# Kernel tuning notes

Measured on AMD Instinct MI355X. Metric: run time of the kernel, lower is better.

Reference implementation:

```python
import jax, jax.numpy as jnp
import numpy as np

B, T, D, L, K = 4, 2048, 2048, 2048, 4  # batch, seq, width, lru_width, conv temporal width


def setup_inputs() -> dict:
    key = jax.random.key(0)
    ks = jax.random.split(key, 12)
    s = 0.02
    f32 = jnp.float32
    return {
        "x": jax.random.normal(ks[0], (B, T, D), f32),
        "w_y": jax.random.normal(ks[1], (D, L), f32) * s,
        "b_y": jnp.zeros((L,), f32),
        "w_x": jax.random.normal(ks[2], (D, L), f32) * s,
        "b_x": jnp.zeros((L,), f32),
        "conv_w": jax.random.normal(ks[3], (K, L), f32) * s,
        "conv_b": jnp.zeros((L,), f32),
        "a_param": jax.random.uniform(ks[4], (L,), f32, 0.5, 4.0),
        "w_ig": jax.random.normal(ks[5], (L, L), f32) * s,
        "b_ig": jnp.zeros((L,), f32),
        "w_ag": jax.random.normal(ks[6], (L, L), f32) * s,
        "b_ag": jnp.zeros((L,), f32),
        "w_out": jax.random.normal(ks[7], (L, D), f32) * s,
        "b_out": jnp.zeros((D,), f32),
    }


def reference(x, w_y, b_y, w_x, b_x, conv_w, conv_b, a_param,
              w_ig, b_ig, w_ag, b_ag, w_out, b_out):
    # x: [B, T, D] (batch_first=True)
    Tn = x.shape[1]
    # gate branch: GELU(linear_y(x))
    y = jax.nn.gelu(jnp.einsum('btd,dl->btl', x, w_y) + b_y, approximate=False)
    # recurrent branch: linear_x -> causal depthwise conv1d (width K)
    xb = jnp.einsum('btd,dl->btl', x, w_x) + b_x
    xp = jnp.pad(xb, ((0, 0), (K - 1, 0), (0, 0)))  # zero left pad (fresh cache)
    conv = conv_b
    for k in range(K):  # y_t = b + sum_k w[k] * x_{t-(K-1-k)}
        conv = conv + conv_w[k] * xp[:, k:k + Tn]
    # RG-LRU
    gate_x = jax.nn.sigmoid(jnp.einsum('btl,lm->btm', conv, w_ig) + b_ig)
    gate_a = jax.nn.sigmoid(jnp.einsum('btl,lm->btm', conv, w_ag) + b_ag)
    log_a = -8.0 * gate_a * jax.nn.softplus(a_param)  # [B,T,L]
    a = jnp.exp(log_a)
    mult = jnp.sqrt(1.0 - jnp.exp(2.0 * log_a))
    reset = (jnp.arange(Tn) == 0)[None, :, None]  # reset at sequence start
    a = jnp.where(reset, 0.0, a)
    mult = jnp.where(reset, 1.0, mult)
    nx = gate_x * conv * mult
    # linear diagonal scan h_t = a_t * h_{t-1} + nx_t
    def step(h, inp):
        a_t, x_t = inp
        h = a_t * h + x_t
        return h, h
    h0 = jnp.zeros((x.shape[0], a.shape[-1]), x.dtype)
    hn, hs = jax.lax.scan(step, h0, (a.transpose(1, 0, 2), nx.transpose(1, 0, 2)))
    h_seq = hs.transpose(1, 0, 2)  # [B,T,L]
    out = jnp.einsum('btl,ld->btd', h_seq * y, w_out) + b_out
    return out, hn
```

## Files before the change

kernel.cpp:

```cpp
#include <hip/hip_runtime.h>
#include <math.h>

#define B_ 4
#define T_ 2048
#define D_ 2048
#define L_ 2048
#define KW 4
#define M_ (B_*T_)

typedef unsigned short u16;
typedef unsigned short u16x8 __attribute__((ext_vector_type(8)));
typedef __bf16 bf16x8 __attribute__((ext_vector_type(8)));
typedef float f32x4 __attribute__((ext_vector_type(4)));

__device__ __forceinline__ u16 f2bf(float f) {
    unsigned u = __float_as_uint(f);
    u += 0x7fffu + ((u >> 16) & 1u);
    return (u16)(u >> 16);
}
__device__ __forceinline__ float bf2f(u16 h) {
    return __uint_as_float(((unsigned)h) << 16);
}
__device__ __forceinline__ float gelu_exact(float v) {
    return 0.5f * v * (1.0f + erff(v * 0.70710678118654752440f));
}
__device__ __forceinline__ float sigmoidf_(float v) {
    return 1.0f / (1.0f + __expf(-v));
}
__device__ __forceinline__ void gload16(const void* g, void* l) {
    __builtin_amdgcn_global_load_lds(
        (const __attribute__((address_space(1))) void*)g,
        (__attribute__((address_space(3))) void*)l,
        16, 0, 0);
}
__device__ __forceinline__ void bar() {
    __builtin_amdgcn_s_barrier();
}

__global__ __launch_bounds__(256)
void castx_kernel(const float* __restrict__ in, u16* __restrict__ out)
{
    const int i = blockIdx.x * 256 + threadIdx.x;
    float4 v = ((const float4*)in)[i];
    ushort4 o;
    o.x = f2bf(v.x); o.y = f2bf(v.y); o.z = f2bf(v.z); o.w = f2bf(v.w);
    ((ushort4*)out)[i] = o;
}

__global__ __launch_bounds__(256)
void transcast_kernel(const float* __restrict__ in, u16* __restrict__ out,
                      int Kd, int Nd)
{
    __shared__ float tile[32][33];
    const int bx = blockIdx.x;
    const int by = blockIdx.y;
    const int tx = threadIdx.x & 31;
    const int ty = threadIdx.x >> 5;
    #pragma unroll
    for (int j = 0; j < 4; ++j) {
        const int r = by*32 + ty + j*8;
        tile[ty + j*8][tx] = in[(size_t)r * Nd + bx*32 + tx];
    }
    __syncthreads();
    #pragma unroll
    for (int j = 0; j < 4; ++j) {
        const int n = bx*32 + ty + j*8;
        out[(size_t)n * Kd + by*32 + tx] = f2bf(tile[tx][ty + j*8]);
    }
}

__device__ __forceinline__ void store_out(float* C, size_t idx, float v) { C[idx] = v; }
__device__ __forceinline__ void store_out(u16*   C, size_t idx, float v) { C[idx] = f2bf(v); }

template<int EPI, typename OutT>
__global__ __launch_bounds__(512, 4)
void mgemm_kernel(const u16* __restrict__ A, const u16* __restrict__ BT,
                  const float* __restrict__ bias, OutT* __restrict__ C,
                  int M, int N, int K,
                  const u16* __restrict__ auxA,
                  const u16* __restrict__ auxC,
                  const float* __restrict__ ap)
{
    __shared__ __align__(16) u16 lds[36864];
    u16* ldsB = lds + 24576;

    const int tid  = threadIdx.x;
    const int wave = tid >> 6;
    const int lane = tid & 63;

    const int nbx = N >> 7;
    const int nwg = nbx * (M >> 8);
    const int bid = blockIdx.x;
    const int li  = (bid & 7) * (nwg >> 3) + (bid >> 3);
    const int bm  = (li / nbx) * 256;
    const int bn  = (li % nbx) * 128;

    const int wr = wave >> 1;
    const int wn = wave & 1;
    const int lr = lane & 15;
    const int q  = lane >> 4;

    const int grow  = lane >> 2;
    const int gslot = (lane & 3) ^ ((lane >> 3) & 3);
    const u16* gA0 = A  + (size_t)(bm + wave*16     + grow) * K + gslot*8;
    const u16* gA1 = A  + (size_t)(bm + (wave+8)*16 + grow) * K + gslot*8;
    const u16* gB0 = BT + (size_t)(bn + wave*16     + grow) * K + gslot*8;
    const int dA0 = wave*512     + lane*8;
    const int dA1 = (wave+8)*512 + lane*8;
    const int dB0 = wave*512     + lane*8;

    auto STAGE = [&](int g) {
        const int s = g % 3;
        const size_t kg = (size_t)g << 5;
        u16* a = lds  + s*8192;
        u16* b = ldsB + s*4096;
        gload16(gA0 + kg, &a[dA0]);
        gload16(gA1 + kg, &a[dA1]);
        gload16(gB0 + kg, &b[dB0]);
    };

    const int ksw = (q ^ ((lr >> 1) & 3)) * 8;

    f32x4 acc[4][4] = {};

    STAGE(0); STAGE(1);
    asm volatile("s_waitcnt vmcnt(3)" ::: "memory");
    bar();

    const int NT = K >> 5;
    for (int g = 0; g < NT; ++g) {
        const int s = g % 3;
        const u16* Ab = lds  + s*8192;
        const u16* Bb = ldsB + s*4096;

        bf16x8 a[4], b[4];
        #pragma unroll
        for (int i = 0; i < 4; ++i)
            a[i] = *(const bf16x8*)&Ab[(wr*64 + i*16 + lr)*32 + ksw];
        #pragma unroll
        for (int j = 0; j < 4; ++j)
            b[j] = *(const bf16x8*)&Bb[(wn*64 + j*16 + lr)*32 + ksw];

        if (g + 2 < NT) STAGE(g + 2);

        __builtin_amdgcn_s_setprio(1);
        #pragma unroll
        for (int i = 0; i < 4; ++i)
            #pragma unroll
            for (int j = 0; j < 4; ++j)
                acc[i][j] = __builtin_amdgcn_mfma_f32_16x16x32_bf16(a[i], b[j], acc[i][j], 0, 0, 0);
        __builtin_amdgcn_s_setprio(0);

        if (g + 2 < NT)      { asm volatile("s_waitcnt vmcnt(3)" ::: "memory"); }
        else if (g + 1 < NT) { asm volatile("s_waitcnt vmcnt(0)" ::: "memory"); }
        bar();
    }

    const int orow = (lane >> 4) * 4;
    float bv[4], spv[4];
    #pragma unroll
    for (int nj = 0; nj < 4; ++nj) {
        const int col = bn + wn*64 + nj*16 + lr;
        bv[nj] = bias[col];
        if (EPI == 3) spv[nj] = log1pf(expf(ap[col]));
    }
    #pragma unroll
    for (int mi = 0; mi < 4; ++mi) {
        #pragma unroll
        for (int r = 0; r < 4; ++r) {
            const int row = bm + wr*64 + mi*16 + orow + r;
            const size_t rb = (size_t)row * N + bn + wn*64 + lr;
            const int t = row & (T_ - 1);
            #pragma unroll
            for (int nj = 0; nj < 4; ++nj) {
                float v = acc[mi][nj][r] + bv[nj];
                if (EPI == 1) {
                    v = gelu_exact(v);
                } else if (EPI == 3) {
                    const float g2 = sigmoidf_(v);
                    v = (t == 0) ? 0.f : expf(-8.0f * g2 * spv[nj]);
                } else if (EPI == 4) {
                    const float gx = sigmoidf_(v);
                    const float av = bf2f(auxA[rb + nj*16]);
                    const float cv = bf2f(auxC[rb + nj*16]);
                    v = gx * cv * sqrtf(fmaxf(0.f, 1.0f - av*av));
                }
                store_out(C, rb + nj*16, v);
            }
        }
    }
}

__global__ __launch_bounds__(256)
void conv_kernel(const u16* __restrict__ xb, const float* __restrict__ cw,
                 const float* __restrict__ cb, u16* __restrict__ out)
{
    const int idx = blockIdx.x * 256 + threadIdx.x;
    const int NL8 = L_ / 8;
    const int l = (idx % NL8) * 8;
    const int bt = idx / NL8;
    const int t = bt & (T_ - 1);
    float acc[8];
    #pragma unroll
    for (int j = 0; j < 8; ++j) acc[j] = cb[l + j];
    #pragma unroll
    for (int k = 0; k < KW; ++k) {
        const int ts = t - (KW-1) + k;
        if (ts >= 0) {
            u16x8 xv = *(const u16x8*)(xb + ((size_t)(bt - (KW-1-k))) * L_ + l);
            #pragma unroll
            for (int j = 0; j < 8; ++j)
                acc[j] = fmaf(cw[k*L_ + l + j], bf2f(xv[j]), acc[j]);
        }
    }
    u16x8 o;
    #pragma unroll
    for (int j = 0; j < 8; ++j) o[j] = f2bf(acc[j]);
    *(u16x8*)(out + (size_t)bt * L_ + l) = o;
}

#define CHUNKS 32
#define CLEN (T_ / CHUNKS)

__global__ __launch_bounds__(256)
void scan1_kernel(const u16* __restrict__ Ab, const u16* __restrict__ Xb,
                  float* __restrict__ Pb, float* __restrict__ Sb)
{
    const int l = blockIdx.x * 256 + threadIdx.x;
    const int c = blockIdx.y;
    const int b = blockIdx.z;
    size_t base = ((size_t)b * T_ + (size_t)c * CLEN) * L_ + l;
    float h = 0.f, P = 1.f;
    #pragma unroll 4
    for (int t = 0; t < CLEN; ++t) {
        float a = bf2f(Ab[base + (size_t)t * L_]);
        float x = bf2f(Xb[base + (size_t)t * L_]);
        h = fmaf(a, h, x);
        P *= a;
    }
    const size_t o = ((size_t)b * CHUNKS + c) * L_ + l;
    Pb[o] = P;
    Sb[o] = h;
}

__global__ __launch_bounds__(256)
void scan2_kernel(const float* __restrict__ Pb, const float* __restrict__ Sb,
                  float* __restrict__ Hin, float* __restrict__ hn)
{
    const int idx = blockIdx.x * 256 + threadIdx.x;
    const int l = idx & (L_ - 1);
    const int b = idx >> 11;
    float h = 0.f;
    for (int c = 0; c < CHUNKS; ++c) {
        const size_t o = ((size_t)b * CHUNKS + c) * L_ + l;
        Hin[o] = h;
        h = fmaf(Pb[o], h, Sb[o]);
    }
    hn[(size_t)b * L_ + l] = h;
}

__global__ __launch_bounds__(256)
void scan3_kernel(const u16* __restrict__ Ab, const u16* __restrict__ Xb,
                  const float* __restrict__ Hin, const u16* __restrict__ Yb,
                  u16* __restrict__ Zb)
{
    const int l = blockIdx.x * 256 + threadIdx.x;
    const int c = blockIdx.y;
    const int b = blockIdx.z;
    float h = Hin[((size_t)b * CHUNKS + c) * L_ + l];
    size_t base = ((size_t)b * T_ + (size_t)c * CLEN) * L_ + l;
    #pragma unroll 4
    for (int t = 0; t < CLEN; ++t) {
        const size_t o = base + (size_t)t * L_;
        h = fmaf(bf2f(Ab[o]), h, bf2f(Xb[o]));
        Zb[o] = f2bf(h * bf2f(Yb[o]));
    }
}

extern "C" void kernel_launch(void* const* d_in, const int* in_sizes, int n_in,
                              void* d_out, int out_size, void* d_ws, size_t ws_size,
                              hipStream_t stream)
{
    const float* x     = (const float*)d_in[0];
    const float* w_y   = (const float*)d_in[1];
    const float* b_y   = (const float*)d_in[2];
    const float* w_x   = (const float*)d_in[3];
    const float* b_x   = (const float*)d_in[4];
    const float* cw    = (const float*)d_in[5];
    const float* cb    = (const float*)d_in[6];
    const float* ap    = (const float*)d_in[7];
    const float* w_ig  = (const float*)d_in[8];
    const float* b_ig  = (const float*)d_in[9];
    const float* w_ag  = (const float*)d_in[10];
    const float* b_ag  = (const float*)d_in[11];
    const float* w_out = (const float*)d_in[12];
    const float* b_out = (const float*)d_in[13];

    float* out = (float*)d_out;
    float* hn  = out + (size_t)M_ * D_;

    const size_t MB = 1u << 20;
    char* w = (char*)d_ws;
    u16*  xbf   = (u16*)(w + 0);
    u16*  wigb  = (u16*)(w + 0);
    u16*  wagb  = (u16*)(w + 8*MB);
    u16*  zb    = (u16*)(w + 0);
    u16*  ybf   = (u16*)(w + 32*MB);
    u16*  xbbf  = (u16*)(w + 64*MB);
    u16*  woutb = (u16*)(w + 64*MB);
    float* Pb   = (float*)(w + 72*MB);
    float* Sb   = (float*)(w + 73*MB);
    float* Hin  = (float*)(w + 74*MB);
    u16*  wyb   = (u16*)(w + 96*MB);
    u16*  wxb   = (u16*)(w + 104*MB);
    u16*  convb = (u16*)(w + 96*MB);
    u16*  abuf  = (u16*)(w + 128*MB);
    u16*  nxbuf = (u16*)(w + 160*MB);

    const dim3 blk(256);
    const dim3 blkG(512);
    const dim3 gG((L_/128) * (M_/256));
    const dim3 gT(2048/32, 2048/32);
    const int  gE8 = (M_ * L_ / 8) / 256;
    const dim3 gScan(L_/256, CHUNKS, B_);
    const u16* nu = nullptr;

    hipLaunchKernelGGL(castx_kernel, dim3((M_*D_/4)/256), blk, 0, stream, x, xbf);
    hipLaunchKernelGGL(transcast_kernel, gT, blk, 0, stream, w_y, wyb, D_, L_);
    hipLaunchKernelGGL(transcast_kernel, gT, blk, 0, stream, w_x, wxb, D_, L_);
    hipLaunchKernelGGL((mgemm_kernel<1, u16>), gG, blkG, 0, stream,
                       xbf, wyb, b_y, ybf, M_, L_, D_, nu, nu, (const float*)nullptr);
    hipLaunchKernelGGL((mgemm_kernel<0, u16>), gG, blkG, 0, stream,
                       xbf, wxb, b_x, xbbf, M_, L_, D_, nu, nu, (const float*)nullptr);
    hipLaunchKernelGGL(transcast_kernel, gT, blk, 0, stream, w_ig, wigb, L_, L_);
    hipLaunchKernelGGL(transcast_kernel, gT, blk, 0, stream, w_ag, wagb, L_, L_);
    hipLaunchKernelGGL(conv_kernel, dim3(gE8), blk, 0, stream, xbbf, cw, cb, convb);
    hipLaunchKernelGGL(transcast_kernel, gT, blk, 0, stream, w_out, woutb, L_, D_);
    hipLaunchKernelGGL((mgemm_kernel<3, u16>), gG, blkG, 0, stream,
                       convb, wagb, b_ag, abuf, M_, L_, L_, nu, nu, ap);
    hipLaunchKernelGGL((mgemm_kernel<4, u16>), gG, blkG, 0, stream,
                       convb, wigb, b_ig, nxbuf, M_, L_, L_, abuf, convb, (const float*)nullptr);
    hipLaunchKernelGGL(scan1_kernel, gScan, blk, 0, stream, abuf, nxbuf, Pb, Sb);
    hipLaunchKernelGGL(scan2_kernel, dim3(B_*L_/256), blk, 0, stream, Pb, Sb, Hin, hn);
    hipLaunchKernelGGL(scan3_kernel, gScan, blk, 0, stream, abuf, nxbuf, Hin, ybf, zb);
    hipLaunchKernelGGL((mgemm_kernel<0, float>), gG, blkG, 0, stream,
                       zb, woutb, b_out, out, M_, D_, L_, nu, nu, (const float*)nullptr);
}
```

Baseline: 523.2 us.

## Double-buffer MFMA register fragments to overlap LDS reads with matrix math

```diff
diff --git a/kernel.cpp b/kernel.cpp
--- a/kernel.cpp
+++ b/kernel.cpp
@@ -73,7 +73,7 @@
 __device__ __forceinline__ void store_out(u16*   C, size_t idx, float v) { C[idx] = f2bf(v); }
 
 template<int EPI, typename OutT>
-__global__ __launch_bounds__(512, 4)
+__global__ __launch_bounds__(512)
 void mgemm_kernel(const u16* __restrict__ A, const u16* __restrict__ BT,
                   const float* __restrict__ bias, OutT* __restrict__ C,
                   int M, int N, int K,
@@ -122,39 +122,54 @@
     const int ksw = (q ^ ((lr >> 1) & 3)) * 8;
 
     f32x4 acc[4][4] = {};
-
-    STAGE(0); STAGE(1);
-    asm volatile("s_waitcnt vmcnt(3)" ::: "memory");
-    bar();
-
-    const int NT = K >> 5;
-    for (int g = 0; g < NT; ++g) {
+    bf16x8 aP[4], bP[4], aQ[4], bQ[4];
+
+    auto LDFRAG = [&](int g, bf16x8 (&af)[4], bf16x8 (&bf)[4]) {
         const int s = g % 3;
         const u16* Ab = lds  + s*8192;
         const u16* Bb = ldsB + s*4096;
-
-        bf16x8 a[4], b[4];
         #pragma unroll
         for (int i = 0; i < 4; ++i)
-            a[i] = *(const bf16x8*)&Ab[(wr*64 + i*16 + lr)*32 + ksw];
+            af[i] = *(const bf16x8*)&Ab[(wr*64 + i*16 + lr)*32 + ksw];
         #pragma unroll
         for (int j = 0; j < 4; ++j)
-            b[j] = *(const bf16x8*)&Bb[(wn*64 + j*16 + lr)*32 + ksw];
-
-        if (g + 2 < NT) STAGE(g + 2);
-
+            bf[j] = *(const bf16x8*)&Bb[(wn*64 + j*16 + lr)*32 + ksw];
+    };
+
+    auto MM = [&](bf16x8 (&af)[4], bf16x8 (&bf)[4]) {
         __builtin_amdgcn_s_setprio(1);
         #pragma unroll
         for (int i = 0; i < 4; ++i)
             #pragma unroll
             for (int j = 0; j < 4; ++j)
-                acc[i][j] = __builtin_amdgcn_mfma_f32_16x16x32_bf16(a[i], b[j], acc[i][j], 0, 0, 0);
+                acc[i][j] = __builtin_amdgcn_mfma_f32_16x16x32_bf16(af[i], bf[j], acc[i][j], 0, 0, 0);
         __builtin_amdgcn_s_setprio(0);
-
-        if (g + 2 < NT)      { asm volatile("s_waitcnt vmcnt(3)" ::: "memory"); }
-        else if (g + 1 < NT) { asm volatile("s_waitcnt vmcnt(0)" ::: "memory"); }
-        bar();
-    }
+    };
+
+    const int NT = K >> 5;
+
+    STAGE(0); STAGE(1);
+    asm volatile("s_waitcnt vmcnt(3)" ::: "memory");
+    bar();
+    LDFRAG(0, aP, bP);
+
+    #define BODY(GG, CURA, CURB, NXTA, NXTB)                                  \
+    {                                                                         \
+        const int gg = (GG);                                                  \
+        if (gg + 2 < NT) STAGE(gg + 2);                                       \
+        if (gg + 2 < NT)      { asm volatile("s_waitcnt vmcnt(3)" ::: "memory"); } \
+        else if (gg + 1 < NT) { asm volatile("s_waitcnt vmcnt(0)" ::: "memory"); } \
+        bar();                                                                \
+        if (gg + 1 < NT) LDFRAG(gg + 1, NXTA, NXTB);                          \
+        MM(CURA, CURB);                                                       \
+        bar();                                                                \
+    }
+
+    for (int g = 0; g < NT; g += 2) {
+        BODY(g,     aP, bP, aQ, bQ);
+        BODY(g + 1, aQ, bQ, aP, bP);
+    }
+    #undef BODY
 
     const int orow = (lane >> 4) * 4;
     float bv[4], spv[4];
```

After: 596.7 us. 14.1% more time.

## Give each GEMM wave private LDS tiles and drop block barriers

Applied to the files above, without the earlier changes.

```diff
diff --git a/kernel.cpp b/kernel.cpp
--- a/kernel.cpp
+++ b/kernel.cpp
@@ -33,9 +33,6 @@
         (__attribute__((address_space(3))) void*)l,
         16, 0, 0);
 }
-__device__ __forceinline__ void bar() {
-    __builtin_amdgcn_s_barrier();
-}
 
 __global__ __launch_bounds__(256)
 void castx_kernel(const float* __restrict__ in, u16* __restrict__ out)
@@ -73,7 +70,7 @@
 __device__ __forceinline__ void store_out(u16*   C, size_t idx, float v) { C[idx] = f2bf(v); }
 
 template<int EPI, typename OutT>
-__global__ __launch_bounds__(512, 4)
+__global__ __launch_bounds__(512)
 void mgemm_kernel(const u16* __restrict__ A, const u16* __restrict__ BT,
                   const float* __restrict__ bias, OutT* __restrict__ C,
                   int M, int N, int K,
@@ -81,8 +78,7 @@
                   const u16* __restrict__ auxC,
                   const float* __restrict__ ap)
 {
-    __shared__ __align__(16) u16 lds[36864];
-    u16* ldsB = lds + 24576;
+    __shared__ __align__(16) u16 lds[65536];
 
     const int tid  = threadIdx.x;
     const int wave = tid >> 6;
@@ -102,46 +98,47 @@
 
     const int grow  = lane >> 2;
     const int gslot = (lane & 3) ^ ((lane >> 3) & 3);
-    const u16* gA0 = A  + (size_t)(bm + wave*16     + grow) * K + gslot*8;
-    const u16* gA1 = A  + (size_t)(bm + (wave+8)*16 + grow) * K + gslot*8;
-    const u16* gB0 = BT + (size_t)(bn + wave*16     + grow) * K + gslot*8;
-    const int dA0 = wave*512     + lane*8;
-    const int dA1 = (wave+8)*512 + lane*8;
-    const int dB0 = wave*512     + lane*8;
+
+    const u16* gA[4]; const u16* gB[4];
+    #pragma unroll
+    for (int c = 0; c < 4; ++c) {
+        gA[c] = A  + (size_t)(bm + wr*64 + c*16 + grow) * K + gslot*8;
+        gB[c] = BT + (size_t)(bn + wn*64 + c*16 + grow) * K + gslot*8;
+    }
+    u16* wbase = lds + wave * 8192;
 
     auto STAGE = [&](int g) {
-        const int s = g % 3;
+        u16* s = wbase + (g & 1) * 4096;
         const size_t kg = (size_t)g << 5;
-        u16* a = lds  + s*8192;
-        u16* b = ldsB + s*4096;
-        gload16(gA0 + kg, &a[dA0]);
-        gload16(gA1 + kg, &a[dA1]);
-        gload16(gB0 + kg, &b[dB0]);
+        #pragma unroll
+        for (int c = 0; c < 4; ++c) {
+            gload16(gA[c] + kg, &s[c*512 + lane*8]);
+            gload16(gB[c] + kg, &s[2048 + c*512 + lane*8]);
+        }
     };
 
     const int ksw = (q ^ ((lr >> 1) & 3)) * 8;
 
     f32x4 acc[4][4] = {};
 
-    STAGE(0); STAGE(1);
-    asm volatile("s_waitcnt vmcnt(3)" ::: "memory");
-    bar();
-
+    STAGE(0);
     const int NT = K >> 5;
     for (int g = 0; g < NT; ++g) {
-        const int s = g % 3;
-        const u16* Ab = lds  + s*8192;
-        const u16* Bb = ldsB + s*4096;
-
+        if (g + 1 < NT) {
+            STAGE(g + 1);
+            asm volatile("s_waitcnt vmcnt(8)" ::: "memory");
+        } else {
+            asm volatile("s_waitcnt vmcnt(0)" ::: "memory");
+        }
+
+        const u16* s = wbase + (g & 1) * 4096;
         bf16x8 a[4], b[4];
         #pragma unroll
         for (int i = 0; i < 4; ++i)
-            a[i] = *(const bf16x8*)&Ab[(wr*64 + i*16 + lr)*32 + ksw];
+            a[i] = *(const bf16x8*)&s[(i*16 + lr)*32 + ksw];
         #pragma unroll
         for (int j = 0; j < 4; ++j)
-            b[j] = *(const bf16x8*)&Bb[(wn*64 + j*16 + lr)*32 + ksw];
-
-        if (g + 2 < NT) STAGE(g + 2);
+            b[j] = *(const bf16x8*)&s[2048 + (j*16 + lr)*32 + ksw];
 
         __builtin_amdgcn_s_setprio(1);
         #pragma unroll
@@ -150,10 +147,6 @@
             for (int j = 0; j < 4; ++j)
                 acc[i][j] = __builtin_amdgcn_mfma_f32_16x16x32_bf16(a[i], b[j], acc[i][j], 0, 0, 0);
         __builtin_amdgcn_s_setprio(0);
-
-        if (g + 2 < NT)      { asm volatile("s_waitcnt vmcnt(3)" ::: "memory"); }
-        else if (g + 1 < NT) { asm volatile("s_waitcnt vmcnt(0)" ::: "memory"); }
-        bar();
     }
 
     const int orow = (lane >> 4) * 4;
```

New measurement: 736.1 us. 40.7% more time.
